# Kernel tuning notes

Measured on AMD Instinct MI355X. Metric: run time of the kernel, lower is better.

## Reference

```python
import jax, jax.numpy as jnp
import numpy as np

D_MODEL = 1024
N_HEADS = 16
HEAD_DIM = D_MODEL // N_HEADS
D_C = 128
THETA = 10000.0


def rope_cos_sin(timestamps):
    # timestamps: (B, L) -> cos, sin: (B, L, HEAD_DIM)
    freqs = 1.0 / (THETA ** (jnp.arange(0, HEAD_DIM, 2, dtype=jnp.float32) / HEAD_DIM))
    t = timestamps[..., None] * freqs            # (B, L, HEAD_DIM//2)
    emb = jnp.concatenate([t, t], axis=-1)       # (B, L, HEAD_DIM)
    return jnp.cos(emb), jnp.sin(emb)


def rotate_half(x):
    x1, x2 = jnp.split(x, 2, axis=-1)
    return jnp.concatenate([-x2, x1], axis=-1)


def setup_inputs() -> dict:
    key = jax.random.key(0)
    ks = jax.random.split(key, 10)
    B, L = 2, 2048
    s = 0.02
    return {
        "query": jax.random.normal(ks[0], (B, L, D_MODEL), jnp.float32),
        "timestamps_q": jax.random.uniform(ks[1], (B, L), jnp.float32) * 365.0,
        "timestamps_kv": jax.random.uniform(ks[2], (B, L), jnp.float32) * 365.0,
        "w_kv_c": jax.random.normal(ks[3], (D_MODEL, D_C), jnp.float32) * s,
        "w_kc_up": jax.random.normal(ks[4], (D_C, D_MODEL), jnp.float32) * s,
        "w_vc_up": jax.random.normal(ks[5], (D_C, D_MODEL), jnp.float32) * s,
        "w_qr": jax.random.normal(ks[6], (D_MODEL, D_MODEL), jnp.float32) * s,
        "w_kr": jax.random.normal(ks[7], (D_MODEL, D_MODEL), jnp.float32) * s,
        "w_o": jax.random.normal(ks[8], (D_MODEL, D_MODEL), jnp.float32) * s,
    }


def reference(query, timestamps_q, timestamps_kv, w_kv_c, w_kc_up, w_vc_up, w_qr, w_kr, w_o):
    B, Lq, _ = query.shape
    key_value = query  # self-attention path (key_value defaults to query)
    Lk = key_value.shape[1]

    def heads(x, L):  # (B, L, D) -> (B, H, L, hd)
        return x.reshape(B, L, N_HEADS, HEAD_DIM).transpose(0, 2, 1, 3)

    c_kv = key_value @ w_kv_c                      # (B, Lk, d_c) low-rank KV
    k_c = heads(c_kv @ w_kc_up, Lk)
    v_c = heads(c_kv @ w_vc_up, Lk)
    q_r = heads(query @ w_qr, Lq)
    k_r = heads(key_value @ w_kr, Lk)

    cos_q, _ = rope_cos_sin(timestamps_q)
    cos_k, _ = rope_cos_sin(timestamps_kv)
    cos_q = cos_q[:, None]                          # (B, 1, Lq, hd)
    cos_k = cos_k[:, None]                          # (B, 1, Lk, hd)
    # Faithful to original (which passes cos_k in the `sin` slot):
    q_r = q_r * cos_q + rotate_half(q_r) * cos_k
    k_r = k_r * cos_q + rotate_half(k_r) * cos_k

    scale = HEAD_DIM ** -0.5
    qs = q_r * scale
    attn = jnp.einsum("bhqd,bhkd->bhqk", qs, k_c) + jnp.einsum("bhqd,bhkd->bhqk", qs, k_r)
    attn_weights = jax.nn.softmax(attn, axis=-1)
    out = jnp.einsum("bhqk,bhkd->bhqd", attn_weights, v_c)
    out = out.transpose(0, 2, 1, 3).reshape(B, Lq, D_MODEL)
    return out @ w_o
```

## Files before the change

### kernel.cpp

```cpp
#include <hip/hip_runtime.h>

typedef float          f32x4    __attribute__((ext_vector_type(4)));
typedef float          f32x2    __attribute__((ext_vector_type(2)));
typedef float          float8v  __attribute__((ext_vector_type(8)));
typedef unsigned short ushort8v __attribute__((ext_vector_type(8)));
typedef unsigned short ushort4v __attribute__((ext_vector_type(4)));
typedef __bf16         bf16x8   __attribute__((ext_vector_type(8)));

__device__ __forceinline__ unsigned short f2b(float x) {
  union { __bf16 b; unsigned short u; } v;
  v.b = (__bf16)x;
  return v.u;
}
__device__ __forceinline__ float b2f(unsigned short h) {
  union { unsigned u; float f; } v; v.u = ((unsigned)h) << 16;
  return v.f;
}

__device__ __forceinline__ void g2lds16(const unsigned short* g,
                                        unsigned short* l) {
  __builtin_amdgcn_global_load_lds(
      (const __attribute__((address_space(1))) unsigned int*)g,
      (__attribute__((address_space(3))) unsigned int*)l, 16, 0, 0);
}

__global__ __launch_bounds__(256) void prep_kernel(
    const float* __restrict__ X, unsigned short* __restrict__ Xb, int cvtb,
    int n8,
    const float* __restrict__ w0, unsigned short* __restrict__ t0,
    const float* __restrict__ w1, unsigned short* __restrict__ t1,
    const float* __restrict__ w2, unsigned short* __restrict__ t2,
    const float* __restrict__ w3, unsigned short* __restrict__ t3,
    const float* __restrict__ w4, unsigned short* __restrict__ t4,
    const float* __restrict__ w5, unsigned short* __restrict__ t5,
    const float* __restrict__ tq, const float* __restrict__ tk,
    f32x2* __restrict__ ctab) {
  __shared__ unsigned short T[64 * 72];
  const int tid = threadIdx.x;
  int blk = blockIdx.x;
  if (blk < cvtb) {
    int i = blk * 256 + tid;
    if (i >= n8) return;
    float8v v = reinterpret_cast<const float8v*>(X)[i];
    ushort8v h;
#pragma unroll
    for (int j = 0; j < 8; ++j) h[j] = f2b(v[j]);
    reinterpret_cast<ushort8v*>(Xb)[i] = h;
    return;
  }
  blk -= cvtb;
  if (blk >= 864) {
    int idx = (blk - 864) * 256 + tid;
    int row = idx >> 5, i = idx & 31;
    float f = exp2f(-(float)i * (13.287712379549449f / 32.f));
    f32x2 c;
    c[0] = cosf(tq[row] * f);
    c[1] = cosf(tk[row] * f);
    ctab[idx] = c;
    return;
  }
  const float* W; unsigned short* WT; int K, N, bx, by;
  if (blk < 256)      { W = w0; WT = t0; K = 1024; N = 1024; bx = blk & 15;         by = blk >> 4; }
  else if (blk < 512) { W = w1; WT = t1; K = 1024; N = 1024; bx = (blk - 256) & 15; by = (blk - 256) >> 4; }
  else if (blk < 544) { W = w2; WT = t2; K = 1024; N = 128;  bx = (blk - 512) & 1;  by = (blk - 512) >> 1; }
  else if (blk < 576) { W = w3; WT = t3; K = 128;  N = 1024; bx = (blk - 544) & 15; by = (blk - 544) >> 4; }
  else if (blk < 608) { W = w4; WT = t4; K = 128;  N = 1024; bx = (blk - 576) & 15; by = (blk - 576) >> 4; }
  else                { W = w5; WT = t5; K = 1024; N = 1024; bx = (blk - 608) & 15; by = (blk - 608) >> 4; }
  const int n0 = bx * 64, k0 = by * 64;
#pragma unroll
  for (int it = 0; it < 2; ++it) {
    int c = tid + it * 256;
    int r = c >> 3, cc = c & 7;
    float8v v = *reinterpret_cast<const float8v*>(
        &W[(size_t)(k0 + r) * N + n0 + cc * 8]);
    ushort8v h;
#pragma unroll
    for (int j = 0; j < 8; ++j) h[j] = f2b(v[j]);
    *reinterpret_cast<ushort8v*>(&T[r * 72 + cc * 8]) = h;
  }
  __syncthreads();
#pragma unroll
  for (int it = 0; it < 2; ++it) {
    int c = tid + it * 256;
    int n = c >> 3, kc = c & 7;
    ushort8v y;
#pragma unroll
    for (int j = 0; j < 8; ++j) y[j] = T[(kc * 8 + j) * 72 + n];
    *reinterpret_cast<ushort8v*>(&WT[(size_t)(n0 + n) * K + k0 + kc * 8]) = y;
  }
}

template <int TM, typename CT, bool ACC>
__global__ __launch_bounds__(256) void gemm_bt(
    const unsigned short* __restrict__ A, const unsigned short* __restrict__ Bt,
    CT* __restrict__ C, int M, int N, int K) {
  static_assert(TM == 64, "vmcnt literal assumes TM=64");
  __shared__ unsigned short As[2][TM * 64];
  __shared__ unsigned short Bs[2][128 * 64];
  const int tid = threadIdx.x;
  const int id = blockIdx.x, cpx = gridDim.x >> 3;
  const int swz = (id & 7) * cpx + (id >> 3);
  const int nwx = N / 128;
  const int m0 = (swz / nwx) * TM, n0 = (swz % nwx) * 128;
  const int wave = tid >> 6, lane = tid & 63;
  const int wm = (wave >> 1) * (TM / 2), wn = (wave & 1) * 64;
  const int l16 = lane & 15, quad = lane >> 4;
  constexpr int MI = TM / 32;

  f32x4 acc[MI][4];
#pragma unroll
  for (int i = 0; i < MI; ++i)
#pragma unroll
    for (int j = 0; j < 4; ++j)
#pragma unroll
      for (int r = 0; r < 4; ++r) acc[i][j][r] = 0.f;

  auto stage = [&](int k0, int b) {
#pragma unroll
    for (int it = 0; it < TM * 8 / 256; ++it) {
      int c = it * 256 + tid;
      int m = c >> 3, kc = (c & 7) ^ (m & 7);
      g2lds16(&A[(size_t)(m0 + m) * K + k0 + kc * 8], &As[b][c * 8]);
    }
#pragma unroll
    for (int it = 0; it < 4; ++it) {
      int c = it * 256 + tid;
      int n = c >> 3, kc = (c & 7) ^ (n & 7);
      g2lds16(&Bt[(size_t)(n0 + n) * K + k0 + kc * 8], &Bs[b][c * 8]);
    }
  };

  const int T = K / 64;
  stage(0, 0);
  for (int t = 0; t < T; ++t) {
    __builtin_amdgcn_s_barrier();
    asm volatile("" ::: "memory");
    if (t + 1 < T) {
      stage((t + 1) * 64, (t + 1) & 1);
      asm volatile("s_waitcnt vmcnt(6)" ::: "memory");
    } else {
      asm volatile("s_waitcnt vmcnt(0)" ::: "memory");
    }
    __builtin_amdgcn_s_barrier();
    asm volatile("" ::: "memory");
    const int cb = t & 1;

#pragma unroll
    for (int ks = 0; ks < 2; ++ks) {
      bf16x8 af[MI], bfr[4];
#pragma unroll
      for (int mi = 0; mi < MI; ++mi) {
        int m = wm + mi * 16 + l16;
        af[mi] = *reinterpret_cast<const bf16x8*>(
            &As[cb][(m * 8 + ((ks * 4 + quad) ^ (m & 7))) * 8]);
      }
#pragma unroll
      for (int ni = 0; ni < 4; ++ni) {
        int n = wn + ni * 16 + l16;
        bfr[ni] = *reinterpret_cast<const bf16x8*>(
            &Bs[cb][(n * 8 + ((ks * 4 + quad) ^ (n & 7))) * 8]);
      }
#pragma unroll
      for (int mi = 0; mi < MI; ++mi)
#pragma unroll
        for (int ni = 0; ni < 4; ++ni)
          acc[mi][ni] = __builtin_amdgcn_mfma_f32_16x16x32_bf16(
              af[mi], bfr[ni], acc[mi][ni], 0, 0, 0);
    }
  }

#pragma unroll
  for (int mi = 0; mi < MI; ++mi)
#pragma unroll
    for (int ni = 0; ni < 4; ++ni) {
      int row = m0 + wm + mi * 16 + quad * 4;
      int col = n0 + wn + ni * 16 + l16;
#pragma unroll
      for (int r = 0; r < 4; ++r) {
        size_t idx = (size_t)(row + r) * N + col;
        float val = acc[mi][ni][r];
        if constexpr (sizeof(CT) == 2) {
          if constexpr (ACC) val += b2f(C[idx]);
          C[idx] = f2b(val);
        } else {
          if constexpr (ACC) val += C[idx];
          C[idx] = val;
        }
      }
    }
}

__global__ __launch_bounds__(256) void gemm_fused3(
    const unsigned short* __restrict__ A, const unsigned short* __restrict__ Bt,
    unsigned short* __restrict__ Cq, unsigned short* __restrict__ Ck,
    unsigned short* __restrict__ Cc, const f32x2* __restrict__ ctab, int K) {
  __shared__ unsigned short As[2][1024 * 8];
  __shared__ unsigned short Bs[2][1024 * 8];
  const int tid = threadIdx.x;
  const int id = blockIdx.x;
  const int swz = (id & 7) * 68 + (id >> 3);
  const int m0 = (swz / 17) * 128, n0 = (swz % 17) * 128;
  const int wave = tid >> 6, lane = tid & 63;
  const int wm = (wave >> 1) * 64, wn = (wave & 1) * 64;
  const int l16 = lane & 15, quad = lane >> 4;

  f32x4 acc[4][4];
#pragma unroll
  for (int i = 0; i < 4; ++i)
#pragma unroll
    for (int j = 0; j < 4; ++j)
#pragma unroll
      for (int r = 0; r < 4; ++r) acc[i][j][r] = 0.f;

  auto stage = [&](int k0, int b) {
#pragma unroll
    for (int it = 0; it < 4; ++it) {
      int c = it * 256 + tid;
      int m = c >> 3, kc = (c & 7) ^ (m & 7);
      g2lds16(&A[(size_t)(m0 + m) * K + k0 + kc * 8], &As[b][c * 8]);
    }
#pragma unroll
    for (int it = 0; it < 4; ++it) {
      int c = it * 256 + tid;
      int n = c >> 3, kc = (c & 7) ^ (n & 7);
      g2lds16(&Bt[(size_t)(n0 + n) * K + k0 + kc * 8], &Bs[b][c * 8]);
    }
  };

  const int T = K / 64;
  stage(0, 0);
  for (int t = 0; t < T; ++t) {
    __builtin_amdgcn_s_barrier();
    asm volatile("" ::: "memory");
    if (t + 1 < T) {
      stage((t + 1) * 64, (t + 1) & 1);
      asm volatile("s_waitcnt vmcnt(8)" ::: "memory");
    } else {
      asm volatile("s_waitcnt vmcnt(0)" ::: "memory");
    }
    __builtin_amdgcn_s_barrier();
    asm volatile("" ::: "memory");
    const int cb = t & 1;

#pragma unroll
    for (int ks = 0; ks < 2; ++ks) {
      bf16x8 af[4], bfr[4];
#pragma unroll
      for (int mi = 0; mi < 4; ++mi) {
        int m = wm + mi * 16 + l16;
        af[mi] = *reinterpret_cast<const bf16x8*>(
            &As[cb][(m * 8 + ((ks * 4 + quad) ^ (m & 7))) * 8]);
      }
#pragma unroll
      for (int ni = 0; ni < 4; ++ni) {
        int n = wn + ni * 16 + l16;
        bfr[ni] = *reinterpret_cast<const bf16x8*>(
            &Bs[cb][(n * 8 + ((ks * 4 + quad) ^ (n & 7))) * 8]);
      }
#pragma unroll
      for (int mi = 0; mi < 4; ++mi)
#pragma unroll
        for (int ni = 0; ni < 4; ++ni)
          acc[mi][ni] = __builtin_amdgcn_mfma_f32_16x16x32_bf16(
              af[mi], bfr[ni], acc[mi][ni], 0, 0, 0);
    }
  }

  if (n0 < 2048) {
    const bool isq = (n0 < 1024);
    unsigned short* dst = isq ? Cq : Ck;
    const int cb = isq ? 0 : 1024;
    const float s = isq ? 0.18033688011112042f : 1.0f;
#pragma unroll
    for (int mi = 0; mi < 4; ++mi)
#pragma unroll
      for (int r = 0; r < 4; ++r) {
        int row = m0 + wm + mi * 16 + quad * 4 + r;
        const f32x2* crow = &ctab[(size_t)row * 32];
#pragma unroll
        for (int np = 0; np < 2; ++np) {
          f32x2 cc = crow[np * 16 + l16];
          float v1 = acc[mi][np][r], v2 = acc[mi][np + 2][r];
          int col = n0 - cb + wn + np * 16 + l16;
          dst[(size_t)row * 1024 + col]      = f2b((v1 * cc[0] - v2 * cc[1]) * s);
          dst[(size_t)row * 1024 + col + 32] = f2b((v2 * cc[0] + v1 * cc[1]) * s);
        }
      }
  } else {
#pragma unroll
    for (int mi = 0; mi < 4; ++mi)
#pragma unroll
      for (int ni = 0; ni < 4; ++ni) {
        int row = m0 + wm + mi * 16 + quad * 4;
        int col = n0 - 2048 + wn + ni * 16 + l16;
#pragma unroll
        for (int r = 0; r < 4; ++r)
          Cc[(size_t)(row + r) * 128 + col] = f2b(acc[mi][ni][r]);
      }
  }
}

__global__ __launch_bounds__(256) void gemm_fused2(
    const unsigned short* __restrict__ A, const unsigned short* __restrict__ Bt,
    unsigned short* __restrict__ Ck, unsigned short* __restrict__ vt, int K) {
  __shared__ unsigned short As[2][1024 * 8];
  __shared__ unsigned short Bs[2][1024 * 8];
  const int tid = threadIdx.x;
  const int id = blockIdx.x;
  const int swz = (id & 7) * 64 + (id >> 3);
  const int m0 = (swz >> 4) * 128, n0 = (swz & 15) * 128;
  const int wave = tid >> 6, lane = tid & 63;
  const int wm = (wave >> 1) * 64, wn = (wave & 1) * 64;
  const int l16 = lane & 15, quad = lane >> 4;

  f32x4 acc[4][4];
#pragma unroll
  for (int i = 0; i < 4; ++i)
#pragma unroll
    for (int j = 0; j < 4; ++j)
#pragma unroll
      for (int r = 0; r < 4; ++r) acc[i][j][r] = 0.f;

  auto stage = [&](int k0, int b) {
#pragma unroll
    for (int it = 0; it < 4; ++it) {
      int c = it * 256 + tid;
      int m = c >> 3, kc = (c & 7) ^ (m & 7);
      g2lds16(&A[(size_t)(m0 + m) * K + k0 + kc * 8], &As[b][c * 8]);
    }
#pragma unroll
    for (int it = 0; it < 4; ++it) {
      int c = it * 256 + tid;
      int n = c >> 3, kc = (c & 7) ^ (n & 7);
      g2lds16(&Bt[(size_t)(n0 + n) * K + k0 + kc * 8], &Bs[b][c * 8]);
    }
  };

  const int T = K / 64;
  stage(0, 0);
  for (int t = 0; t < T; ++t) {
    __builtin_amdgcn_s_barrier();
    asm volatile("" ::: "memory");
    if (t + 1 < T) {
      stage((t + 1) * 64, (t + 1) & 1);
      asm volatile("s_waitcnt vmcnt(8)" ::: "memory");
    } else {
      asm volatile("s_waitcnt vmcnt(0)" ::: "memory");
    }
    __builtin_amdgcn_s_barrier();
    asm volatile("" ::: "memory");
    const int cb = t & 1;

#pragma unroll
    for (int ks = 0; ks < 2; ++ks) {
      bf16x8 af[4], bfr[4];
#pragma unroll
      for (int mi = 0; mi < 4; ++mi) {
        int m = wm + mi * 16 + l16;
        af[mi] = *reinterpret_cast<const bf16x8*>(
            &As[cb][(m * 8 + ((ks * 4 + quad) ^ (m & 7))) * 8]);
      }
#pragma unroll
      for (int ni = 0; ni < 4; ++ni) {
        int n = wn + ni * 16 + l16;
        bfr[ni] = *reinterpret_cast<const bf16x8*>(
            &Bs[cb][(n * 8 + ((ks * 4 + quad) ^ (n & 7))) * 8]);
      }
#pragma unroll
      for (int mi = 0; mi < 4; ++mi)
#pragma unroll
        for (int ni = 0; ni < 4; ++ni)
          acc[mi][ni] = __builtin_amdgcn_mfma_f32_16x16x32_bf16(
              af[mi], bfr[ni], acc[mi][ni], 0, 0, 0);
    }
  }

  if (n0 < 1024) {
#pragma unroll
    for (int mi = 0; mi < 4; ++mi)
#pragma unroll
      for (int ni = 0; ni < 4; ++ni) {
        int row = m0 + wm + mi * 16 + quad * 4;
        int col = n0 + wn + ni * 16 + l16;
#pragma unroll
        for (int r = 0; r < 4; ++r) {
          size_t idx = (size_t)(row + r) * 1024 + col;
          Ck[idx] = f2b(acc[mi][ni][r] + b2f(Ck[idx]));
        }
      }
  } else {
    const int L = 2048;
#pragma unroll
    for (int mi = 0; mi < 4; ++mi)
#pragma unroll
      for (int ni = 0; ni < 4; ++ni) {
        int row = m0 + wm + mi * 16 + quad * 4;
        int col = n0 - 1024 + wn + ni * 16 + l16;
        int l = row & (L - 1);
        int bh = ((row >> 11) << 4) | (col >> 6);
        int d = col & 63;
        int s = (l & ~63) | (((l >> 5) & 1) << 5) | (((l >> 3) & 1) << 4) |
                (((l >> 2) & 1) << 3) | (((l >> 4) & 1) << 2);
        ushort4v w;
#pragma unroll
        for (int r = 0; r < 4; ++r) w[r] = f2b(acc[mi][ni][r]);
        *reinterpret_cast<ushort4v*>(
            &vt[(size_t)bh * 64 * L + (size_t)d * L + s]) = w;
      }
  }
}

__global__ __launch_bounds__(256, 3) void flash17_kernel(
    const unsigned short* __restrict__ qs, const unsigned short* __restrict__ ks,
    const unsigned short* __restrict__ vt, unsigned short* __restrict__ o,
    int L) {
  __shared__ unsigned short Ks[3][512 * 8];
  __shared__ unsigned short Vs[3][512 * 8];
  const int tid = threadIdx.x;
  const int wave = tid >> 6, lane = tid & 63;
  const int l16 = lane & 15, quad = lane >> 4;
  const int bh = blockIdx.y;
  const int qb = blockIdx.x * 128 + wave * 32;
  const size_t base = ((size_t)(bh >> 4) * L) * 1024 + (bh & 15) * 64;
  const size_t vtbase = (size_t)bh * 64 * L;

  bf16x8 aq[2][2];
#pragma unroll
  for (int mt = 0; mt < 2; ++mt) {
    size_t qrow = base + (size_t)(qb + mt * 16 + l16) * 1024;
    aq[mt][0] = *reinterpret_cast<const bf16x8*>(&qs[qrow + quad * 8]);
    aq[mt][1] = *reinterpret_cast<const bf16x8*>(&qs[qrow + 32 + quad * 8]);
  }

  ushort8v onesu;
#pragma unroll
  for (int j = 0; j < 8; ++j) onesu[j] = 0x3F80;
  bf16x8 ones = *reinterpret_cast<bf16x8*>(&onesu);

  f32x4 oacc[2][4];
  f32x4 lacc[2];
#pragma unroll
  for (int mt = 0; mt < 2; ++mt) {
#pragma unroll
    for (int r = 0; r < 4; ++r) lacc[mt][r] = 0.f;
#pragma unroll
    for (int nt = 0; nt < 4; ++nt)
#pragma unroll
      for (int r = 0; r < 4; ++r) oacc[mt][nt][r] = 0.f;
  }

  auto stage = [&](int t, int b) {
    int k0 = t * 64;
#pragma unroll
    for (int it = 0; it < 2; ++it) {
      int c = it * 256 + tid;
      int key = c >> 3, dc = (c & 7) ^ (key & 7);
      g2lds16(&ks[base + (size_t)(k0 + key) * 1024 + dc * 8], &Ks[b][c * 8]);
    }
#pragma unroll
    for (int it = 0; it < 2; ++it) {
      int c = it * 256 + tid;
      int d = c >> 3, kc = (c & 7) ^ (d & 7);
      g2lds16(&vt[vtbase + (size_t)d * L + k0 + kc * 8], &Vs[b][c * 8]);
    }
  };

  const int T = L / 64;
  stage(0, 0);
  stage(1, 1);

  for (int t = 0; t < T; ++t) {
    __builtin_amdgcn_s_barrier();
    asm volatile("" ::: "memory");
    if (t + 2 < T) stage(t + 2, (t + 2) % 3);
    if (t + 2 < T)
      asm volatile("s_waitcnt vmcnt(8)" ::: "memory");
    else if (t + 1 < T)
      asm volatile("s_waitcnt vmcnt(4)" ::: "memory");
    else
      asm volatile("s_waitcnt vmcnt(0)" ::: "memory");
    __builtin_amdgcn_s_barrier();
    asm volatile("" ::: "memory");

    const int cb = t % 3;
    const unsigned short* Kb = &Ks[cb][0];
    const unsigned short* Vb = &Vs[cb][0];

    f32x4 st[2][4];
#pragma unroll
    for (int nt = 0; nt < 4; ++nt) {
      int key = nt * 16 + l16;
      int dc0 = quad ^ (key & 7);
      int dc1 = (4 + quad) ^ (key & 7);
      bf16x8 bk0 = *reinterpret_cast<const bf16x8*>(&Kb[(key * 8 + dc0) * 8]);
      bf16x8 bk1 = *reinterpret_cast<const bf16x8*>(&Kb[(key * 8 + dc1) * 8]);
#pragma unroll
      for (int mt = 0; mt < 2; ++mt) {
        f32x4 z; z[0] = z[1] = z[2] = z[3] = 0.f;
        z = __builtin_amdgcn_mfma_f32_16x16x32_bf16(bk0, aq[mt][0], z, 0, 0, 0);
        z = __builtin_amdgcn_mfma_f32_16x16x32_bf16(bk1, aq[mt][1], z, 0, 0, 0);
        st[mt][nt] = z;
      }
    }

    bf16x8 ap[2][2];
#pragma unroll
    for (int mt = 0; mt < 2; ++mt) {
#pragma unroll
      for (int hf = 0; hf < 2; ++hf)
#pragma unroll
        for (int w = 0; w < 4; ++w) {
          int nt = 2 * hf + (w >> 1), p = w & 1;
          ap[mt][hf][2 * w] =
              (__bf16)__builtin_amdgcn_exp2f(st[mt][nt][2 * p]);
          ap[mt][hf][2 * w + 1] =
              (__bf16)__builtin_amdgcn_exp2f(st[mt][nt][2 * p + 1]);
        }
      lacc[mt] = __builtin_amdgcn_mfma_f32_16x16x32_bf16(ap[mt][0], ones,
                                                         lacc[mt], 0, 0, 0);
      lacc[mt] = __builtin_amdgcn_mfma_f32_16x16x32_bf16(ap[mt][1], ones,
                                                         lacc[mt], 0, 0, 0);
    }

#pragma unroll
    for (int nt = 0; nt < 4; ++nt) {
      int d = nt * 16 + l16;
#pragma unroll
      for (int hf = 0; hf < 2; ++hf) {
        int kc = (hf * 4 + quad) ^ (d & 7);
        bf16x8 bv = *reinterpret_cast<const bf16x8*>(&Vb[(d * 8 + kc) * 8]);
#pragma unroll
        for (int mt = 0; mt < 2; ++mt)
          oacc[mt][nt] = __builtin_amdgcn_mfma_f32_16x16x32_bf16(
              ap[mt][hf], bv, oacc[mt][nt], 0, 0, 0);
      }
    }
  }

#pragma unroll
  for (int mt = 0; mt < 2; ++mt)
#pragma unroll
    for (int r = 0; r < 4; ++r) {
      float inv = __builtin_amdgcn_rcpf(lacc[mt][r]);
      int q = qb + mt * 16 + quad * 4 + r;
#pragma unroll
      for (int nt = 0; nt < 4; ++nt)
        o[base + (size_t)q * 1024 + nt * 16 + l16] =
            f2b(oacc[mt][nt][r] * inv);
    }
}

extern "C" void kernel_launch(void* const* d_in, const int* in_sizes, int n_in,
                              void* d_out, int out_size, void* d_ws, size_t ws_size,
                              hipStream_t stream) {
  const float* X    = (const float*)d_in[0];
  const float* tq   = (const float*)d_in[1];
  const float* tk   = (const float*)d_in[2];
  const float* wkvc = (const float*)d_in[3];
  const float* wkc  = (const float*)d_in[4];
  const float* wvc  = (const float*)d_in[5];
  const float* wqr  = (const float*)d_in[6];
  const float* wkr  = (const float*)d_in[7];
  const float* wo   = (const float*)d_in[8];

  const int D = 1024, DC = 128, L = 2048;
  const int M = in_sizes[0] / D;
  const int B = M / L;
  const int NBH = B * 16;
  (void)n_in; (void)out_size; (void)ws_size;

  unsigned short* p = (unsigned short*)d_ws;
  auto take = [&](size_t n) { unsigned short* r = p; p += n; return r; };
  unsigned short* Xb    = take((size_t)M * D);
  unsigned short* qsb   = take((size_t)M * D);
  unsigned short* ksb   = take((size_t)M * D);
  unsigned short* vcb   = take((size_t)M * D);
  unsigned short* ckv   = take((size_t)M * DC);
  unsigned short* Wbig  = take((size_t)(2 * D + DC) * D);
  unsigned short* Wkcvc = take((size_t)(2 * D) * DC);
  unsigned short* WoT   = take((size_t)D * D);
  f32x2* ctab = (f32x2*)take((size_t)M * 32 * 4);
  unsigned short* vtb   = Xb;
  unsigned short* obuf  = vcb;

  const int n8 = M * D / 8;
  const int cvtb = (n8 + 255) / 256;
  const int ropeb = M / 8;
  prep_kernel<<<cvtb + 864 + ropeb, 256, 0, stream>>>(
      X, Xb, cvtb, n8,
      wqr,  Wbig,
      wkr,  Wbig + (size_t)D * D,
      wkvc, Wbig + (size_t)2 * D * D,
      wkc,  Wkcvc,
      wvc,  Wkcvc + (size_t)D * DC,
      wo,   WoT,
      tq, tk, ctab);

  {
    gemm_fused3<<<(2 * D + DC) / 128 * (M / 128), 256, 0, stream>>>(
        Xb, Wbig, qsb, ksb, ckv, ctab, D);
  }
  {
    gemm_fused2<<<(2 * D / 128) * (M / 128), 256, 0, stream>>>(
        ckv, Wkcvc, ksb, vtb, DC);
  }

  dim3 fg(L / 128, NBH);
  flash17_kernel<<<fg, 256, 0, stream>>>(qsb, ksb, vtb, obuf, L);

  {
    gemm_bt<64, float, false><<<(D / 128) * (M / 64), 256, 0, stream>>>(
        obuf, WoT, (float*)d_out, M, D, D);
  }
}
```

Before: 193.0 us.

## Use 128-key tiles with double buffering and raise priority around PV MFMAs

The flash attention kernel now processes 128 keys per iteration instead of 64. It moves from a triple-buffered to a double-buffered LDS pipeline, which halves the number of barriers and loop iterations. The V tile layout gets a two-group swizzle, and s_setprio wraps the PV MFMA block so waves in that phase get scheduling priority. LDS per block grows and launch bounds drop to 2 blocks per CU, so occupancy falls and there is less prefetch depth to hide latency.

```diff
diff --git a/kernel.cpp b/kernel.cpp
--- a/kernel.cpp
+++ b/kernel.cpp
@@ -410,12 +410,12 @@
   }
 }
 
-__global__ __launch_bounds__(256, 3) void flash17_kernel(
+__global__ __launch_bounds__(256, 2) void flash18_kernel(
     const unsigned short* __restrict__ qs, const unsigned short* __restrict__ ks,
     const unsigned short* __restrict__ vt, unsigned short* __restrict__ o,
     int L) {
-  __shared__ unsigned short Ks[3][512 * 8];
-  __shared__ unsigned short Vs[3][512 * 8];
+  __shared__ unsigned short Ks[2][1024 * 8];
+  __shared__ unsigned short Vs[2][1024 * 8];
   const int tid = threadIdx.x;
   const int wave = tid >> 6, lane = tid & 63;
   const int l16 = lane & 15, quad = lane >> 4;
@@ -450,91 +450,97 @@
   }
 
   auto stage = [&](int t, int b) {
-    int k0 = t * 64;
-#pragma unroll
-    for (int it = 0; it < 2; ++it) {
+    int k0 = t * 128;
+#pragma unroll
+    for (int it = 0; it < 4; ++it) {
       int c = it * 256 + tid;
       int key = c >> 3, dc = (c & 7) ^ (key & 7);
       g2lds16(&ks[base + (size_t)(k0 + key) * 1024 + dc * 8], &Ks[b][c * 8]);
     }
 #pragma unroll
-    for (int it = 0; it < 2; ++it) {
-      int c = it * 256 + tid;
-      int d = c >> 3, kc = (c & 7) ^ (d & 7);
-      g2lds16(&vt[vtbase + (size_t)d * L + k0 + kc * 8], &Vs[b][c * 8]);
+    for (int it = 0; it < 4; ++it) {
+      int c = it * 256 + tid;
+      int d = c >> 4, oc = c & 15;
+      int g = oc >> 3, oo = oc & 7;
+      int kcs = g * 8 + (oo ^ (d & 7));
+      g2lds16(&vt[vtbase + (size_t)d * L + k0 + kcs * 8], &Vs[b][c * 8]);
     }
   };
 
-  const int T = L / 64;
+  const int T = L / 128;
   stage(0, 0);
-  stage(1, 1);
 
   for (int t = 0; t < T; ++t) {
     __builtin_amdgcn_s_barrier();
     asm volatile("" ::: "memory");
-    if (t + 2 < T) stage(t + 2, (t + 2) % 3);
-    if (t + 2 < T)
+    if (t + 1 < T) {
+      stage(t + 1, (t + 1) & 1);
       asm volatile("s_waitcnt vmcnt(8)" ::: "memory");
-    else if (t + 1 < T)
-      asm volatile("s_waitcnt vmcnt(4)" ::: "memory");
-    else
+    } else {
       asm volatile("s_waitcnt vmcnt(0)" ::: "memory");
-    __builtin_amdgcn_s_barrier();
-    asm volatile("" ::: "memory");
-
-    const int cb = t % 3;
+    }
+    __builtin_amdgcn_s_barrier();
+    asm volatile("" ::: "memory");
+
+    const int cb = t & 1;
     const unsigned short* Kb = &Ks[cb][0];
     const unsigned short* Vb = &Vs[cb][0];
 
-    f32x4 st[2][4];
-#pragma unroll
-    for (int nt = 0; nt < 4; ++nt) {
-      int key = nt * 16 + l16;
-      int dc0 = quad ^ (key & 7);
-      int dc1 = (4 + quad) ^ (key & 7);
-      bf16x8 bk0 = *reinterpret_cast<const bf16x8*>(&Kb[(key * 8 + dc0) * 8]);
-      bf16x8 bk1 = *reinterpret_cast<const bf16x8*>(&Kb[(key * 8 + dc1) * 8]);
-#pragma unroll
-      for (int mt = 0; mt < 2; ++mt) {
-        f32x4 z; z[0] = z[1] = z[2] = z[3] = 0.f;
-        z = __builtin_amdgcn_mfma_f32_16x16x32_bf16(bk0, aq[mt][0], z, 0, 0, 0);
-        z = __builtin_amdgcn_mfma_f32_16x16x32_bf16(bk1, aq[mt][1], z, 0, 0, 0);
-        st[mt][nt] = z;
-      }
-    }
-
-    bf16x8 ap[2][2];
-#pragma unroll
-    for (int mt = 0; mt < 2; ++mt) {
-#pragma unroll
-      for (int hf = 0; hf < 2; ++hf)
-#pragma unroll
-        for (int w = 0; w < 4; ++w) {
-          int nt = 2 * hf + (w >> 1), p = w & 1;
-          ap[mt][hf][2 * w] =
-              (__bf16)__builtin_amdgcn_exp2f(st[mt][nt][2 * p]);
-          ap[mt][hf][2 * w + 1] =
-              (__bf16)__builtin_amdgcn_exp2f(st[mt][nt][2 * p + 1]);
+    bf16x8 ap[2][4];
+#pragma unroll
+    for (int g = 0; g < 2; ++g) {
+      f32x4 st[2][4];
+#pragma unroll
+      for (int nt4 = 0; nt4 < 4; ++nt4) {
+        int key = (g * 4 + nt4) * 16 + l16;
+        int dc0 = quad ^ (key & 7);
+        int dc1 = (4 + quad) ^ (key & 7);
+        bf16x8 bk0 = *reinterpret_cast<const bf16x8*>(
+            &Kb[(key * 8 + dc0) * 8]);
+        bf16x8 bk1 = *reinterpret_cast<const bf16x8*>(
+            &Kb[(key * 8 + dc1) * 8]);
+#pragma unroll
+        for (int mt = 0; mt < 2; ++mt) {
+          f32x4 z; z[0] = z[1] = z[2] = z[3] = 0.f;
+          z = __builtin_amdgcn_mfma_f32_16x16x32_bf16(bk0, aq[mt][0], z, 0, 0, 0);
+          z = __builtin_amdgcn_mfma_f32_16x16x32_bf16(bk1, aq[mt][1], z, 0, 0, 0);
+          st[mt][nt4] = z;
         }
-      lacc[mt] = __builtin_amdgcn_mfma_f32_16x16x32_bf16(ap[mt][0], ones,
-                                                         lacc[mt], 0, 0, 0);
-      lacc[mt] = __builtin_amdgcn_mfma_f32_16x16x32_bf16(ap[mt][1], ones,
-                                                         lacc[mt], 0, 0, 0);
-    }
-
+      }
+#pragma unroll
+      for (int mt = 0; mt < 2; ++mt)
+#pragma unroll
+        for (int hfg = 0; hfg < 2; ++hfg) {
+          int kf = g * 2 + hfg;
+#pragma unroll
+          for (int w = 0; w < 4; ++w) {
+            int nt4 = 2 * hfg + (w >> 1), p = w & 1;
+            ap[mt][kf][2 * w] =
+                (__bf16)__builtin_amdgcn_exp2f(st[mt][nt4][2 * p]);
+            ap[mt][kf][2 * w + 1] =
+                (__bf16)__builtin_amdgcn_exp2f(st[mt][nt4][2 * p + 1]);
+          }
+          lacc[mt] = __builtin_amdgcn_mfma_f32_16x16x32_bf16(
+              ap[mt][kf], ones, lacc[mt], 0, 0, 0);
+        }
+    }
+
+    __builtin_amdgcn_s_setprio(1);
 #pragma unroll
     for (int nt = 0; nt < 4; ++nt) {
       int d = nt * 16 + l16;
 #pragma unroll
-      for (int hf = 0; hf < 2; ++hf) {
-        int kc = (hf * 4 + quad) ^ (d & 7);
-        bf16x8 bv = *reinterpret_cast<const bf16x8*>(&Vb[(d * 8 + kc) * 8]);
+      for (int kf = 0; kf < 4; ++kf) {
+        int kc = (kf >> 1) * 8 + (((kf & 1) * 4 + quad) ^ (d & 7));
+        bf16x8 bv = *reinterpret_cast<const bf16x8*>(
+            &Vb[(d * 16 + kc) * 8]);
 #pragma unroll
         for (int mt = 0; mt < 2; ++mt)
           oacc[mt][nt] = __builtin_amdgcn_mfma_f32_16x16x32_bf16(
-              ap[mt][hf], bv, oacc[mt][nt], 0, 0, 0);
-      }
-    }
+              ap[mt][kf], bv, oacc[mt][nt], 0, 0, 0);
+      }
+    }
+    __builtin_amdgcn_s_setprio(0);
   }
 
 #pragma unroll
@@ -606,7 +612,7 @@
   }
 
   dim3 fg(L / 128, NBH);
-  flash17_kernel<<<fg, 256, 0, stream>>>(qsb, ksb, vtb, obuf, L);
+  flash18_kernel<<<fg, 256, 0, stream>>>(qsb, ksb, vtb, obuf, L);
 
   {
     gemm_bt<64, float, false><<<(D / 128) * (M / 64), 256, 0, stream>>>(
```

After: 191.5 us. Within noise of the previous version (-0.8%).
